# Optimization experiments

Hardware: AMD Instinct MI355X
Metric: run time of the kernel (lower is better)

Reference implementation:

```python
import jax, jax.numpy as jnp
import numpy as np

EPS = 1e-6


def setup_inputs() -> dict:
    key = jax.random.key(0)
    k1, _ = jax.random.split(key)
    L, D = 128, 262144
    slots = jax.random.normal(k1, (L, D), dtype=jnp.float32)
    temperature = jnp.ones((), dtype=jnp.float32)  # temperature = 1.0
    return {"slots": slots, "temperature": temperature, "length": L}


def reference(slots, temperature, length):
    # slots: [L, D]; pairwise cosine similarity (torch: x.y / max(|x||y|, eps))
    L = length
    norms = jnp.sqrt(jnp.sum(slots * slots, axis=1))                # [L]
    gram = jnp.einsum('id,jd->ij', slots, slots)                    # [L, L]
    sim = gram / jnp.maximum(norms[:, None] * norms[None, :], EPS)  # [L, L]
    logits = sim / temperature
    E = jnp.exp(logits)                                             # [L, L]
    # denominator for pair (i, j): sum_{k != j} exp(sim(i,k)/T)  (k=i included)
    denom = jnp.sum(E, axis=1, keepdims=True) - E                   # [L, L]
    log_ratio = logits - jnp.log(denom)                             # log(num/den)
    idx = jnp.arange(L)
    penalty = jnp.abs(idx[:, None] - idx[None, :]).astype(slots.dtype)  # |i-j|
    upper = (idx[:, None] < idx[None, :]).astype(slots.dtype)           # i < j
    total = jnp.sum(-log_ratio * penalty * upper)
    # original divides by i*j/2 with final loop values i=j=length-1
    total = total / ((L - 1) * (L - 1) / 2.0)
    return total
```

## Files before the change

### kernel.cpp

```cpp
#include <hip/hip_runtime.h>
#include <hip/hip_bf16.h>

typedef __attribute__((ext_vector_type(8))) short bf16x8;
typedef __attribute__((ext_vector_type(4))) float f32x4;

constexpr int L     = 128;
constexpr int BK    = 64;
constexpr int GRID  = 512;
constexpr int PITCH = BK * 2;

__device__ inline float blo(unsigned w) { unsigned v = w << 16;          return __builtin_bit_cast(float, v); }
__device__ inline float bhi(unsigned w) { unsigned v = w & 0xffff0000u;  return __builtin_bit_cast(float, v); }

__global__ __launch_bounds__(512, 4)
void gram_kernel(const float* __restrict__ slots, uint2* __restrict__ p16,
                 unsigned* __restrict__ counter, int D, int nChunks, int G) {
    __shared__ __align__(16) char lds[2][L * PITCH];
    const int t    = threadIdx.x;
    const int wave = t >> 6;
    const int lane = t & 63;

    if (blockIdx.x == 0 && t == 0) *counter = 0;

    f32x4 acc[8];
#pragma unroll
    for (int c = 0; c < 8; ++c) acc[c] = (f32x4)0.f;

    float4 ld[4];

    auto issue = [&](int chunk) {
#pragma unroll
        for (int q = 0; q < 4; ++q) {
            int idx  = t + 512 * q;
            int row  = idx >> 4;
            int col4 = idx & 15;
            ld[q] = *reinterpret_cast<const float4*>(
                slots + (size_t)row * D + (size_t)chunk * BK + col4 * 4);
        }
    };
    auto commit = [&](int buf) {
#pragma unroll
        for (int q = 0; q < 4; ++q) {
            int idx  = t + 512 * q;
            int row  = idx >> 4;
            int col4 = idx & 15;
            const unsigned* f = reinterpret_cast<const unsigned*>(&ld[q]);
            uint2 w;
            w.x = __builtin_amdgcn_perm(f[1], f[0], 0x07060302u);
            w.y = __builtin_amdgcn_perm(f[3], f[2], 0x07060302u);
            int byte = (col4 * 8) ^ ((row & 7) << 4);
            *reinterpret_cast<uint2*>(&lds[buf][row * PITCH + byte]) = w;
        }
    };
    auto ldfrag = [&](int buf, int row, int kk) -> bf16x8 {
        int byte = row * PITCH + ((kk * 2 + ((lane >> 4) << 4)) ^ ((row & 7) << 4));
        return *reinterpret_cast<const bf16x8*>(&lds[buf][byte]);
    };

    issue(blockIdx.x);
    commit(0);
    __syncthreads();

    int k = 0;
    for (int c = blockIdx.x; c < nChunks; c += G, ++k) {
        const int cur = k & 1;
        const bool more = (c + G < nChunks);
        if (more) issue(c + G);

#pragma unroll
        for (int kk = 0; kk < BK; kk += 32) {
            bf16x8 a = ldfrag(cur, wave * 16 + (lane & 15), kk);
#pragma unroll
            for (int cc = 0; cc < 8; ++cc) {
                bf16x8 b = ldfrag(cur, cc * 16 + (lane & 15), kk);
                acc[cc] = __builtin_amdgcn_mfma_f32_16x16x32_bf16(a, b, acc[cc], 0, 0, 0);
            }
        }

        if (more) commit(cur ^ 1);
        __syncthreads();
    }

    uint2* pb = p16 + (size_t)blockIdx.x * 4096;
#pragma unroll
    for (int cc = 0; cc < 8; ++cc) {
        const unsigned* a = reinterpret_cast<const unsigned*>(&acc[cc]);
        uint2 w;
        w.x = __builtin_amdgcn_perm(a[1], a[0], 0x07060302u);
        w.y = __builtin_amdgcn_perm(a[3], a[2], 0x07060302u);
        pb[cc * 512 + t] = w;
    }
}

__global__ __launch_bounds__(256)
void reduce_finalize(const uint2* __restrict__ p16, float* __restrict__ gram,
                     unsigned* __restrict__ counter,
                     const float* __restrict__ temperature, float* __restrict__ out,
                     int G) {
    __shared__ f32x4 red[8][32];
    __shared__ float norms[L];
    __shared__ float wred[4];
    __shared__ unsigned ticket_s;
    const int t   = threadIdx.x;
    const int sub = t >> 5;
    const int sl  = t & 31;
    const int j   = blockIdx.x * 32 + sl;

    f32x4 s = (f32x4)0.f;
#pragma unroll 8
    for (int b = sub; b < G; b += 8) {
        const uint2 u = p16[(size_t)b * 4096 + j];
        s[0] += blo(u.x); s[1] += bhi(u.x);
        s[2] += blo(u.y); s[3] += bhi(u.y);
    }
    red[sub][sl] = s;
    __syncthreads();
    if (t < 32) {
        f32x4 s4 = red[0][t];
#pragma unroll
        for (int w = 1; w < 8; ++w) s4 += red[w][t];
        const int myj  = blockIdx.x * 32 + t;
        const int cc   = myj >> 9;
        const int tenc = myj & 511;
        const int wv = tenc >> 6, ln = tenc & 63;
        const int growb = wv * 16 + ((ln >> 4) << 2);
        const int gcol  = cc * 16 + (ln & 15);
#pragma unroll
        for (int q = 0; q < 4; ++q) gram[(growb + q) * L + gcol] = s4[q];
    }

    __syncthreads();
    if (t == 0) {
        __threadfence();
        ticket_s = atomicAdd(counter, 1u);
    }
    __syncthreads();
    if (ticket_s != (unsigned)(gridDim.x - 1)) return;
    __threadfence();

    if (t < L) norms[t] = sqrtf(gram[t * L + t]);
    __syncthreads();

    const float invT = 1.0f / temperature[0];
    const int r = t >> 1;
    const int q = t & 1;
    const float ni = norms[r];

    float ps = 0.f;
    for (int jj = q; jj < L; jj += 2) {
        float sim = gram[r * L + jj] / fmaxf(ni * norms[jj], 1e-6f);
        ps += __expf(sim * invT);
    }
    ps += __shfl_xor(ps, 1);
    const float rowsum = ps;

    float tot = 0.f;
    for (int jj = q; jj < L; jj += 2) {
        if (jj > r) {
            float logit = (gram[r * L + jj] / fmaxf(ni * norms[jj], 1e-6f)) * invT;
            tot += -(logit - __logf(rowsum - __expf(logit))) * (float)(jj - r);
        }
    }
#pragma unroll
    for (int m = 1; m < 64; m <<= 1) tot += __shfl_xor(tot, m);
    if ((t & 63) == 0) wred[t >> 6] = tot;
    __syncthreads();
    if (t == 0)
        out[0] = (wred[0] + wred[1] + wred[2] + wred[3]) /
                 ((float)(L - 1) * (float)(L - 1) * 0.5f);
}

extern "C" void kernel_launch(void* const* d_in, const int* in_sizes, int n_in,
                              void* d_out, int out_size, void* d_ws, size_t ws_size,
                              hipStream_t stream) {
    const float* slots       = (const float*)d_in[0];
    const float* temperature = (const float*)d_in[1];
    float* out  = (float*)d_out;

    const int D = in_sizes[0] / L;
    const int nChunks = D / BK;
    int G = GRID;
    if (G > nChunks) G = nChunks;

    uint2*    p16     = (uint2*)d_ws;
    float*    gram    = (float*)((char*)d_ws + (size_t)G * 32768);
    unsigned* counter = (unsigned*)((char*)gram + (size_t)L * L * 4);

    gram_kernel<<<G, 512, 0, stream>>>(slots, p16, counter, D, nChunks, G);
    reduce_finalize<<<128, 256, 0, stream>>>(p16, gram, counter, temperature, out, G);
}
```

Before: 58.87 us.

## Fuse gram and reduce-finalize kernels using atomic tickets and spin-wait

Merges the split-K gram kernel and the reduction/finalize kernel into one launch. The last 128 blocks to finish their partial gram spin-wait until all blocks are done, then each reduces a 32-column slice of the partials. A second ticket counter picks the final block to compute the loss. This removes a kernel launch boundary and its tail gap, but adds a memset launch, a spin-wait that assumes all blocks are co-resident, and idle waiting blocks.

```diff
diff --git a/kernel.cpp b/kernel.cpp
--- a/kernel.cpp
+++ b/kernel.cpp
@@ -13,161 +13,180 @@
 __device__ inline float bhi(unsigned w) { unsigned v = w & 0xffff0000u;  return __builtin_bit_cast(float, v); }
 
 __global__ __launch_bounds__(512, 4)
-void gram_kernel(const float* __restrict__ slots, uint2* __restrict__ p16,
-                 unsigned* __restrict__ counter, int D, int nChunks, int G) {
+void fused_kernel(const float* __restrict__ slots, uint2* __restrict__ p16,
+                  float* __restrict__ gram, unsigned* __restrict__ cnt,
+                  const float* __restrict__ temperature, float* __restrict__ out,
+                  int D, int nChunks, int G) {
     __shared__ __align__(16) char lds[2][L * PITCH];
+    __shared__ unsigned tk1, tk2;
     const int t    = threadIdx.x;
     const int wave = t >> 6;
     const int lane = t & 63;
 
-    if (blockIdx.x == 0 && t == 0) *counter = 0;
-
-    f32x4 acc[8];
-#pragma unroll
-    for (int c = 0; c < 8; ++c) acc[c] = (f32x4)0.f;
-
-    float4 ld[4];
-
-    auto issue = [&](int chunk) {
-#pragma unroll
-        for (int q = 0; q < 4; ++q) {
-            int idx  = t + 512 * q;
-            int row  = idx >> 4;
-            int col4 = idx & 15;
-            ld[q] = *reinterpret_cast<const float4*>(
-                slots + (size_t)row * D + (size_t)chunk * BK + col4 * 4);
-        }
-    };
-    auto commit = [&](int buf) {
-#pragma unroll
-        for (int q = 0; q < 4; ++q) {
-            int idx  = t + 512 * q;
-            int row  = idx >> 4;
-            int col4 = idx & 15;
-            const unsigned* f = reinterpret_cast<const unsigned*>(&ld[q]);
+    {
+        f32x4 acc[8];
+#pragma unroll
+        for (int c = 0; c < 8; ++c) acc[c] = (f32x4)0.f;
+
+        float4 ld[4];
+
+        auto issue = [&](int chunk) {
+#pragma unroll
+            for (int q = 0; q < 4; ++q) {
+                int idx  = t + 512 * q;
+                int row  = idx >> 4;
+                int col4 = idx & 15;
+                ld[q] = *reinterpret_cast<const float4*>(
+                    slots + (size_t)row * D + (size_t)chunk * BK + col4 * 4);
+            }
+        };
+        auto commit = [&](int buf) {
+#pragma unroll
+            for (int q = 0; q < 4; ++q) {
+                int idx  = t + 512 * q;
+                int row  = idx >> 4;
+                int col4 = idx & 15;
+                const unsigned* f = reinterpret_cast<const unsigned*>(&ld[q]);
+                uint2 w;
+                w.x = __builtin_amdgcn_perm(f[1], f[0], 0x07060302u);
+                w.y = __builtin_amdgcn_perm(f[3], f[2], 0x07060302u);
+                int byte = (col4 * 8) ^ ((row & 7) << 4);
+                *reinterpret_cast<uint2*>(&lds[buf][row * PITCH + byte]) = w;
+            }
+        };
+        auto ldfrag = [&](int buf, int row, int kk) -> bf16x8 {
+            int byte = row * PITCH + ((kk * 2 + ((lane >> 4) << 4)) ^ ((row & 7) << 4));
+            return *reinterpret_cast<const bf16x8*>(&lds[buf][byte]);
+        };
+
+        issue(blockIdx.x);
+        commit(0);
+        __syncthreads();
+
+        int k = 0;
+        for (int c = blockIdx.x; c < nChunks; c += G, ++k) {
+            const int cur = k & 1;
+            const bool more = (c + G < nChunks);
+            if (more) issue(c + G);
+
+#pragma unroll
+            for (int kk = 0; kk < BK; kk += 32) {
+                bf16x8 a = ldfrag(cur, wave * 16 + (lane & 15), kk);
+#pragma unroll
+                for (int cc = 0; cc < 8; ++cc) {
+                    bf16x8 b = ldfrag(cur, cc * 16 + (lane & 15), kk);
+                    acc[cc] = __builtin_amdgcn_mfma_f32_16x16x32_bf16(a, b, acc[cc], 0, 0, 0);
+                }
+            }
+
+            if (more) commit(cur ^ 1);
+            __syncthreads();
+        }
+
+        uint2* pb = p16 + (size_t)blockIdx.x * 4096;
+#pragma unroll
+        for (int cc = 0; cc < 8; ++cc) {
+            const unsigned* a = reinterpret_cast<const unsigned*>(&acc[cc]);
             uint2 w;
-            w.x = __builtin_amdgcn_perm(f[1], f[0], 0x07060302u);
-            w.y = __builtin_amdgcn_perm(f[3], f[2], 0x07060302u);
-            int byte = (col4 * 8) ^ ((row & 7) << 4);
-            *reinterpret_cast<uint2*>(&lds[buf][row * PITCH + byte]) = w;
-        }
-    };
-    auto ldfrag = [&](int buf, int row, int kk) -> bf16x8 {
-        int byte = row * PITCH + ((kk * 2 + ((lane >> 4) << 4)) ^ ((row & 7) << 4));
-        return *reinterpret_cast<const bf16x8*>(&lds[buf][byte]);
-    };
-
-    issue(blockIdx.x);
-    commit(0);
-    __syncthreads();
-
-    int k = 0;
-    for (int c = blockIdx.x; c < nChunks; c += G, ++k) {
-        const int cur = k & 1;
-        const bool more = (c + G < nChunks);
-        if (more) issue(c + G);
-
-#pragma unroll
-        for (int kk = 0; kk < BK; kk += 32) {
-            bf16x8 a = ldfrag(cur, wave * 16 + (lane & 15), kk);
-#pragma unroll
-            for (int cc = 0; cc < 8; ++cc) {
-                bf16x8 b = ldfrag(cur, cc * 16 + (lane & 15), kk);
-                acc[cc] = __builtin_amdgcn_mfma_f32_16x16x32_bf16(a, b, acc[cc], 0, 0, 0);
-            }
-        }
-
-        if (more) commit(cur ^ 1);
-        __syncthreads();
-    }
-
-    uint2* pb = p16 + (size_t)blockIdx.x * 4096;
-#pragma unroll
-    for (int cc = 0; cc < 8; ++cc) {
-        const unsigned* a = reinterpret_cast<const unsigned*>(&acc[cc]);
-        uint2 w;
-        w.x = __builtin_amdgcn_perm(a[1], a[0], 0x07060302u);
-        w.y = __builtin_amdgcn_perm(a[3], a[2], 0x07060302u);
-        pb[cc * 512 + t] = w;
-    }
-}
-
-__global__ __launch_bounds__(256)
-void reduce_finalize(const uint2* __restrict__ p16, float* __restrict__ gram,
-                     unsigned* __restrict__ counter,
-                     const float* __restrict__ temperature, float* __restrict__ out,
-                     int G) {
-    __shared__ f32x4 red[8][32];
-    __shared__ float norms[L];
-    __shared__ float wred[4];
-    __shared__ unsigned ticket_s;
-    const int t   = threadIdx.x;
-    const int sub = t >> 5;
-    const int sl  = t & 31;
-    const int j   = blockIdx.x * 32 + sl;
-
-    f32x4 s = (f32x4)0.f;
-#pragma unroll 8
-    for (int b = sub; b < G; b += 8) {
-        const uint2 u = p16[(size_t)b * 4096 + j];
-        s[0] += blo(u.x); s[1] += bhi(u.x);
-        s[2] += blo(u.y); s[3] += bhi(u.y);
-    }
-    red[sub][sl] = s;
-    __syncthreads();
-    if (t < 32) {
-        f32x4 s4 = red[0][t];
-#pragma unroll
-        for (int w = 1; w < 8; ++w) s4 += red[w][t];
-        const int myj  = blockIdx.x * 32 + t;
-        const int cc   = myj >> 9;
-        const int tenc = myj & 511;
-        const int wv = tenc >> 6, ln = tenc & 63;
-        const int growb = wv * 16 + ((ln >> 4) << 2);
-        const int gcol  = cc * 16 + (ln & 15);
-#pragma unroll
-        for (int q = 0; q < 4; ++q) gram[(growb + q) * L + gcol] = s4[q];
+            w.x = __builtin_amdgcn_perm(a[1], a[0], 0x07060302u);
+            w.y = __builtin_amdgcn_perm(a[3], a[2], 0x07060302u);
+            pb[cc * 512 + t] = w;
+        }
     }
 
     __syncthreads();
     if (t == 0) {
         __threadfence();
-        ticket_s = atomicAdd(counter, 1u);
-    }
-    __syncthreads();
-    if (ticket_s != (unsigned)(gridDim.x - 1)) return;
+        tk1 = atomicAdd(&cnt[0], 1u);
+    }
+    __syncthreads();
+    const unsigned rank = tk1;
+    if (rank < (unsigned)(G - 128)) return;
+
+    if (t == 0) {
+        while (atomicAdd(&cnt[0], 0u) < (unsigned)G) __builtin_amdgcn_s_sleep(8);
+    }
+    __syncthreads();
     __threadfence();
 
-    if (t < L) norms[t] = sqrtf(gram[t * L + t]);
-    __syncthreads();
-
-    const float invT = 1.0f / temperature[0];
-    const int r = t >> 1;
-    const int q = t & 1;
-    const float ni = norms[r];
-
-    float ps = 0.f;
-    for (int jj = q; jj < L; jj += 2) {
-        float sim = gram[r * L + jj] / fmaxf(ni * norms[jj], 1e-6f);
-        ps += __expf(sim * invT);
-    }
-    ps += __shfl_xor(ps, 1);
-    const float rowsum = ps;
-
-    float tot = 0.f;
-    for (int jj = q; jj < L; jj += 2) {
-        if (jj > r) {
-            float logit = (gram[r * L + jj] / fmaxf(ni * norms[jj], 1e-6f)) * invT;
-            tot += -(logit - __logf(rowsum - __expf(logit))) * (float)(jj - r);
-        }
-    }
-#pragma unroll
-    for (int m = 1; m < 64; m <<= 1) tot += __shfl_xor(tot, m);
-    if ((t & 63) == 0) wred[t >> 6] = tot;
-    __syncthreads();
-    if (t == 0)
-        out[0] = (wred[0] + wred[1] + wred[2] + wred[3]) /
-                 ((float)(L - 1) * (float)(L - 1) * 0.5f);
+    {
+        f32x4* red = reinterpret_cast<f32x4*>(&lds[0][0]);
+        const int sub = t >> 5;
+        const int sl  = t & 31;
+        const int rr  = (int)rank - (G - 128);
+        const int j   = rr * 32 + sl;
+
+        f32x4 s = (f32x4)0.f;
+#pragma unroll 8
+        for (int b = sub; b < G; b += 16) {
+            const uint2 u = p16[(size_t)b * 4096 + j];
+            s[0] += blo(u.x); s[1] += bhi(u.x);
+            s[2] += blo(u.y); s[3] += bhi(u.y);
+        }
+        red[sub * 32 + sl] = s;
+        __syncthreads();
+        if (t < 32) {
+            f32x4 s4 = red[t];
+#pragma unroll
+            for (int w = 1; w < 16; ++w) s4 += red[w * 32 + t];
+            const int myj  = rr * 32 + t;
+            const int cc   = myj >> 9;
+            const int tenc = myj & 511;
+            const int wv = tenc >> 6, ln = tenc & 63;
+            const int growb = wv * 16 + ((ln >> 4) << 2);
+            const int gcol  = cc * 16 + (ln & 15);
+#pragma unroll
+            for (int q = 0; q < 4; ++q) gram[(growb + q) * L + gcol] = s4[q];
+        }
+    }
+
+    __syncthreads();
+    if (t == 0) {
+        __threadfence();
+        tk2 = atomicAdd(&cnt[32], 1u);
+    }
+    __syncthreads();
+    if (tk2 != 127u) return;
+    __threadfence();
+
+    {
+        float* norms = reinterpret_cast<float*>(&lds[0][0]);
+        float* wred  = norms + L;
+        if (t < L) norms[t] = sqrtf(gram[t * L + t]);
+        __syncthreads();
+
+        const float invT = 1.0f / temperature[0];
+        const int r = t >> 2;
+        const int q = t & 3;
+        const float ni = norms[r];
+
+        float ps = 0.f;
+        for (int jj = q; jj < L; jj += 4) {
+            float sim = gram[r * L + jj] / fmaxf(ni * norms[jj], 1e-6f);
+            ps += __expf(sim * invT);
+        }
+        ps += __shfl_xor(ps, 1);
+        ps += __shfl_xor(ps, 2);
+        const float rowsum = ps;
+
+        float tot = 0.f;
+        for (int jj = q; jj < L; jj += 4) {
+            if (jj > r) {
+                float logit = (gram[r * L + jj] / fmaxf(ni * norms[jj], 1e-6f)) * invT;
+                tot += -(logit - __logf(rowsum - __expf(logit))) * (float)(jj - r);
+            }
+        }
+#pragma unroll
+        for (int m = 1; m < 64; m <<= 1) tot += __shfl_xor(tot, m);
+        if (lane == 0) wred[wave] = tot;
+        __syncthreads();
+        if (t == 0) {
+            float s = 0.f;
+#pragma unroll
+            for (int w = 0; w < 8; ++w) s += wred[w];
+            out[0] = s / ((float)(L - 1) * (float)(L - 1) * 0.5f);
+        }
+    }
 }
 
 extern "C" void kernel_launch(void* const* d_in, const int* in_sizes, int n_in,
@@ -182,10 +201,11 @@
     int G = GRID;
     if (G > nChunks) G = nChunks;
 
-    uint2*    p16     = (uint2*)d_ws;
-    float*    gram    = (float*)((char*)d_ws + (size_t)G * 32768);
-    unsigned* counter = (unsigned*)((char*)gram + (size_t)L * L * 4);
-
-    gram_kernel<<<G, 512, 0, stream>>>(slots, p16, counter, D, nChunks, G);
-    reduce_finalize<<<128, 256, 0, stream>>>(p16, gram, counter, temperature, out, G);
+    uint2*    p16  = (uint2*)d_ws;
+    float*    gram = (float*)((char*)d_ws + (size_t)G * 32768);
+    unsigned* cnt  = (unsigned*)((char*)gram + (size_t)L * L * 4);
+
+    hipMemsetAsync(cnt, 0, 256, stream);
+    fused_kernel<<<G, 512, 0, stream>>>(slots, p16, gram, cnt, temperature, out,
+                                        D, nChunks, G);
 }
```

New measurement: 102.8 us. 74.6% more time.

## Deepen gram prefetch to two chunks ahead and stage gram in LDS for finalize

Applied to the files above, without the earlier changes.

The gram kernel now keeps two register sets of global loads in flight, prefetching two chunks ahead instead of one, and replaces __syncthreads with a barrier that waits only on LDS traffic. The reduce kernel uses 256 blocks of 16 columns with 16-way partial sums instead of 128 blocks of 32 with 8-way. The final block copies the whole 128x128 gram matrix into 64 KB of shared memory before the softmax/log pass. The aim is to hide global-load latency in the main loop and cut repeated global reads in the tail. The cost is more registers per thread and a large shared allocation in the reduce kernel, which may lower occupancy.

```diff
diff --git a/kernel.cpp b/kernel.cpp
--- a/kernel.cpp
+++ b/kernel.cpp
@@ -12,39 +12,45 @@
 __device__ inline float blo(unsigned w) { unsigned v = w << 16;          return __builtin_bit_cast(float, v); }
 __device__ inline float bhi(unsigned w) { unsigned v = w & 0xffff0000u;  return __builtin_bit_cast(float, v); }
 
+__device__ inline void soft_barrier() {
+    asm volatile("s_waitcnt lgkmcnt(0)" ::: "memory");
+    __builtin_amdgcn_s_barrier();
+    __builtin_amdgcn_sched_barrier(0);
+}
+
 __global__ __launch_bounds__(512, 4)
 void gram_kernel(const float* __restrict__ slots, uint2* __restrict__ p16,
-                 unsigned* __restrict__ counter, int D, int nChunks, int G) {
+                 unsigned* __restrict__ cnt, int D, int nChunks, int G) {
     __shared__ __align__(16) char lds[2][L * PITCH];
     const int t    = threadIdx.x;
     const int wave = t >> 6;
     const int lane = t & 63;
 
-    if (blockIdx.x == 0 && t == 0) *counter = 0;
+    if (blockIdx.x == 0 && t == 0) *cnt = 0;
 
     f32x4 acc[8];
 #pragma unroll
     for (int c = 0; c < 8; ++c) acc[c] = (f32x4)0.f;
 
-    float4 ld[4];
-
-    auto issue = [&](int chunk) {
+    float4 ldA[4], ldB[4];
+
+    auto issue = [&](float4 (&dst)[4], int chunk) {
 #pragma unroll
         for (int q = 0; q < 4; ++q) {
             int idx  = t + 512 * q;
             int row  = idx >> 4;
             int col4 = idx & 15;
-            ld[q] = *reinterpret_cast<const float4*>(
+            dst[q] = *reinterpret_cast<const float4*>(
                 slots + (size_t)row * D + (size_t)chunk * BK + col4 * 4);
         }
     };
-    auto commit = [&](int buf) {
+    auto commit = [&](float4 (&src)[4], int buf) {
 #pragma unroll
         for (int q = 0; q < 4; ++q) {
             int idx  = t + 512 * q;
             int row  = idx >> 4;
             int col4 = idx & 15;
-            const unsigned* f = reinterpret_cast<const unsigned*>(&ld[q]);
+            const unsigned* f = reinterpret_cast<const unsigned*>(&src[q]);
             uint2 w;
             w.x = __builtin_amdgcn_perm(f[1], f[0], 0x07060302u);
             w.y = __builtin_amdgcn_perm(f[3], f[2], 0x07060302u);
@@ -57,15 +63,15 @@
         return *reinterpret_cast<const bf16x8*>(&lds[buf][byte]);
     };
 
-    issue(blockIdx.x);
-    commit(0);
-    __syncthreads();
+    issue(ldA, blockIdx.x);
+    if (blockIdx.x + G < nChunks) issue(ldB, blockIdx.x + G);
+    commit(ldA, 0);
+    soft_barrier();
 
     int k = 0;
     for (int c = blockIdx.x; c < nChunks; c += G, ++k) {
         const int cur = k & 1;
-        const bool more = (c + G < nChunks);
-        if (more) issue(c + G);
+        if (c + 2 * G < nChunks) issue(cur == 0 ? ldA : ldB, c + 2 * G);
 
 #pragma unroll
         for (int kk = 0; kk < BK; kk += 32) {
@@ -77,8 +83,8 @@
             }
         }
 
-        if (more) commit(cur ^ 1);
-        __syncthreads();
+        if (c + G < nChunks) commit(cur == 0 ? ldB : ldA, cur ^ 1);
+        soft_barrier();
     }
 
     uint2* pb = p16 + (size_t)blockIdx.x * 4096;
@@ -94,32 +100,33 @@
 
 __global__ __launch_bounds__(256)
 void reduce_finalize(const uint2* __restrict__ p16, float* __restrict__ gram,
-                     unsigned* __restrict__ counter,
+                     unsigned* __restrict__ cnt,
                      const float* __restrict__ temperature, float* __restrict__ out,
                      int G) {
-    __shared__ f32x4 red[8][32];
+    __shared__ __align__(16) float g[L * L];
     __shared__ float norms[L];
     __shared__ float wred[4];
     __shared__ unsigned ticket_s;
     const int t   = threadIdx.x;
-    const int sub = t >> 5;
-    const int sl  = t & 31;
-    const int j   = blockIdx.x * 32 + sl;
+    const int sl  = t & 15;
+    const int sub = t >> 4;
+    const int j   = blockIdx.x * 16 + sl;
 
     f32x4 s = (f32x4)0.f;
 #pragma unroll 8
-    for (int b = sub; b < G; b += 8) {
+    for (int b = sub; b < G; b += 16) {
         const uint2 u = p16[(size_t)b * 4096 + j];
         s[0] += blo(u.x); s[1] += bhi(u.x);
         s[2] += blo(u.y); s[3] += bhi(u.y);
     }
-    red[sub][sl] = s;
-    __syncthreads();
-    if (t < 32) {
-        f32x4 s4 = red[0][t];
-#pragma unroll
-        for (int w = 1; w < 8; ++w) s4 += red[w][t];
-        const int myj  = blockIdx.x * 32 + t;
+    f32x4* red = reinterpret_cast<f32x4*>(g);
+    red[sub * 16 + sl] = s;
+    __syncthreads();
+    if (t < 16) {
+        f32x4 s4 = red[t];
+#pragma unroll
+        for (int w = 1; w < 16; ++w) s4 += red[w * 16 + t];
+        const int myj  = blockIdx.x * 16 + t;
         const int cc   = myj >> 9;
         const int tenc = myj & 511;
         const int wv = tenc >> 6, ln = tenc & 63;
@@ -132,13 +139,20 @@
     __syncthreads();
     if (t == 0) {
         __threadfence();
-        ticket_s = atomicAdd(counter, 1u);
+        ticket_s = atomicAdd(cnt, 1u);
     }
     __syncthreads();
     if (ticket_s != (unsigned)(gridDim.x - 1)) return;
     __threadfence();
 
-    if (t < L) norms[t] = sqrtf(gram[t * L + t]);
+#pragma unroll
+    for (int q = 0; q < 16; ++q) {
+        int i = t + 256 * q;
+        *reinterpret_cast<float4*>(&g[i * 4]) =
+            *reinterpret_cast<const float4*>(&gram[i * 4]);
+    }
+    __syncthreads();
+    if (t < L) norms[t] = sqrtf(g[t * L + t]);
     __syncthreads();
 
     const float invT = 1.0f / temperature[0];
@@ -148,7 +162,7 @@
 
     float ps = 0.f;
     for (int jj = q; jj < L; jj += 2) {
-        float sim = gram[r * L + jj] / fmaxf(ni * norms[jj], 1e-6f);
+        float sim = g[r * L + jj] / fmaxf(ni * norms[jj], 1e-6f);
         ps += __expf(sim * invT);
     }
     ps += __shfl_xor(ps, 1);
@@ -157,7 +171,7 @@
     float tot = 0.f;
     for (int jj = q; jj < L; jj += 2) {
         if (jj > r) {
-            float logit = (gram[r * L + jj] / fmaxf(ni * norms[jj], 1e-6f)) * invT;
+            float logit = (g[r * L + jj] / fmaxf(ni * norms[jj], 1e-6f)) * invT;
             tot += -(logit - __logf(rowsum - __expf(logit))) * (float)(jj - r);
         }
     }
@@ -182,10 +196,10 @@
     int G = GRID;
     if (G > nChunks) G = nChunks;
 
-    uint2*    p16     = (uint2*)d_ws;
-    float*    gram    = (float*)((char*)d_ws + (size_t)G * 32768);
-    unsigned* counter = (unsigned*)((char*)gram + (size_t)L * L * 4);
-
-    gram_kernel<<<G, 512, 0, stream>>>(slots, p16, counter, D, nChunks, G);
-    reduce_finalize<<<128, 256, 0, stream>>>(p16, gram, counter, temperature, out, G);
-}
+    uint2*    p16  = (uint2*)d_ws;
+    float*    gram = (float*)((char*)d_ws + (size_t)G * 32768);
+    unsigned* cnt  = (unsigned*)((char*)gram + (size_t)L * L * 4);
+
+    gram_kernel<<<G, 512, 0, stream>>>(slots, p16, cnt, D, nChunks, G);
+    reduce_finalize<<<256, 256, 0, stream>>>(p16, gram, cnt, temperature, out, G);
+}
```

New measurement: 98.20 us. 1.67x slower.
